# Performance work log

Hardware: AMD Instinct MI355X
Metric: run time of the kernel (lower is better)

The kernel has to match this reference:

```python
import jax, jax.numpy as jnp
import numpy as np

D_MODEL = 1024
EXPAND = 2
INNER = D_MODEL * EXPAND  # 2048
D_STATE = 64
K = 3
BSZ = 2
SEQ = 4096


def setup_inputs() -> dict:
    key = jax.random.key(0)
    ks = jax.random.split(key, 12)
    s = 0.02

    def w(k, shape):
        return jax.random.normal(k, shape, jnp.float32) * s

    return {
        "x": jax.random.normal(ks[0], (BSZ, SEQ, D_MODEL), jnp.float32),
        "W_in": w(ks[1], (D_MODEL, 2 * INNER)),
        "b_in": jnp.zeros((2 * INNER,), jnp.float32),
        "conv_w": w(ks[2], (INNER, K)),            # depthwise kernel per channel
        "conv_b": jnp.zeros((INNER,), jnp.float32),
        "W_dt": w(ks[3], (INNER, D_STATE)),
        "b_dt": jnp.zeros((D_STATE,), jnp.float32),
        "W_B": w(ks[4], (INNER, D_STATE)),
        "b_B": jnp.zeros((D_STATE,), jnp.float32),
        "W_C": w(ks[5], (INNER, D_STATE)),
        "b_C": jnp.zeros((D_STATE,), jnp.float32),
        "W_si": w(ks[6], (D_STATE, INNER)),
        "b_si": jnp.zeros((INNER,), jnp.float32),
        "D": jnp.ones((INNER,), jnp.float32),
        "W_out": w(ks[7], (INNER, D_MODEL)),
        "b_out": jnp.zeros((D_MODEL,), jnp.float32),
    }


def reference(x, W_in, b_in, conv_w, conv_b, W_dt, b_dt, W_B, b_B, W_C, b_C,
              W_si, b_si, D, W_out, b_out):
    bsz, seq_len, _ = x.shape
    inner = W_in.shape[1] // 2
    k = conv_w.shape[1]

    xz = x @ W_in + b_in                      # [B, L, 2*inner]
    x_main, gate = xz[..., :inner], xz[..., inner:]

    # Causal depthwise conv: torch pads k-1 both sides then slices [:L],
    # equivalent to left-pad (k-1), right-pad 0.
    lhs = jnp.transpose(x_main, (0, 2, 1))    # [B, C, L]
    rhs = conv_w[:, None, :]                  # [C, 1, K]
    conv = jax.lax.conv_general_dilated(
        lhs, rhs, window_strides=(1,), padding=[(k - 1, 0)],
        dimension_numbers=("NCH", "OIH", "NCH"), feature_group_count=inner)
    x_main = jnp.transpose(conv, (0, 2, 1)) + conv_b  # [B, L, inner]
    x_main = jax.nn.silu(x_main)

    dt = jax.nn.sigmoid(x_main @ W_dt + b_dt)  # [B, L, d_state]
    Bm = x_main @ W_B + b_B
    Cm = x_main @ W_C + b_C

    # Selective state recurrence: state_t = (1-dt_t)*state_{t-1} + dt_t*B_t
    def step(state, inp):
        dt_t, B_t, C_t = inp                  # each [B, d_state]
        state = (1.0 - dt_t) * state + dt_t * B_t
        return state, C_t * state

    xs = (jnp.moveaxis(dt, 1, 0), jnp.moveaxis(Bm, 1, 0), jnp.moveaxis(Cm, 1, 0))
    state0 = jnp.zeros((bsz, dt.shape[-1]), x.dtype)
    _, y = jax.lax.scan(step, state0, xs)     # [L, B, d_state]
    y = jnp.moveaxis(y, 0, 1)                 # [B, L, d_state]

    # LayerNorm over last dim, no affine, eps=1e-5 (torch F.layer_norm default)
    mu = jnp.mean(y, axis=-1, keepdims=True)
    var = jnp.var(y, axis=-1, keepdims=True)
    y = (y - mu) * jax.lax.rsqrt(var + 1e-5)

    y = y @ W_si + b_si                       # [B, L, inner]
    y = y + D * x_main
    y = y * jax.nn.sigmoid(gate)
    return y @ W_out + b_out                  # [B, L, d_model]
```

## Files before the change

### kernel.cpp

```cpp
#include <hip/hip_runtime.h>
#include <hip/hip_bf16.h>
#include <math.h>


namespace {

typedef __bf16 bf16x8 __attribute__((ext_vector_type(8)));
typedef float  f32x4  __attribute__((ext_vector_type(4)));
typedef unsigned short u16;

constexpr int kSeq = 4096;

__device__ __forceinline__ float sigmoid_f(float x) { return 1.0f / (1.0f + expf(-x)); }
__device__ __forceinline__ u16   f2bf(float f) { __bf16 h = (__bf16)f; return __builtin_bit_cast(u16, h); }
__device__ __forceinline__ float bf2f(u16 u)   { return (float)__builtin_bit_cast(__bf16, u); }

__device__ __forceinline__ void gll16(const u16* g, u16* l) {
    __builtin_amdgcn_global_load_lds(
        (const __attribute__((address_space(1))) unsigned int*)g,
        (__attribute__((address_space(3))) unsigned int*)l,
        16, 0, 0);
}

__device__ __forceinline__ int xcd_swizzle(int lin, int nwg) {
    const int q = nwg >> 3, r = nwg & 7;
    const int xcd = lin & 7, idx = lin >> 3;
    return (xcd < r ? xcd * (q + 1) : r * (q + 1) + (xcd - r) * q) + idx;
}

__global__ __launch_bounds__(256)
void convert_bf16(const float* __restrict__ in, u16* __restrict__ out, long n4)
{
    long i = (long)blockIdx.x * 256 + threadIdx.x;
    if (i >= n4) return;
    float4 v = reinterpret_cast<const float4*>(in)[i];
    ushort4 o = make_ushort4(f2bf(v.x), f2bf(v.y), f2bf(v.z), f2bf(v.w));
    reinterpret_cast<ushort4*>(out)[i] = o;
}

__device__ __forceinline__ void tr_body(float (*tile)[33],
                                        const float* __restrict__ in, u16* __restrict__ out,
                                        int R, int C, int r0, int c0, int t)
{
    const int lr = t >> 3, lc = (t & 7) * 4;
    float4 v = *reinterpret_cast<const float4*>(in + (size_t)(r0 + lr) * C + c0 + lc);
    tile[lr][lc + 0] = v.x; tile[lr][lc + 1] = v.y;
    tile[lr][lc + 2] = v.z; tile[lr][lc + 3] = v.w;
    __syncthreads();
    const int oc = t >> 3, orr = (t & 7) * 4;
    ushort4 o = make_ushort4(f2bf(tile[orr + 0][oc]), f2bf(tile[orr + 1][oc]),
                             f2bf(tile[orr + 2][oc]), f2bf(tile[orr + 3][oc]));
    *reinterpret_cast<ushort4*>(out + (size_t)(c0 + oc) * R + r0 + orr) = o;
}

__global__ __launch_bounds__(256)
void transpose_big(const float* __restrict__ Win, u16* __restrict__ WinT,
                   const float* __restrict__ Wout, u16* __restrict__ WoutT)
{
    __shared__ float tile[32][33];
    const int t = threadIdx.x;
    if (blockIdx.z == 0) {
        tr_body(tile, Win, WinT, 1024, 4096, blockIdx.y * 32, blockIdx.x * 32, t);
    } else {
        if (blockIdx.x >= 64) return;
        tr_body(tile, Wout, WoutT, 2048, 1024, blockIdx.x * 32, blockIdx.y * 32, t);
    }
}

__global__ __launch_bounds__(256)
void transpose_small(const float* __restrict__ Wdt, const float* __restrict__ WB,
                     const float* __restrict__ WC,  const float* __restrict__ Wsi,
                     u16* __restrict__ WdtbcT, u16* __restrict__ WsiT)
{
    __shared__ float tile[32][33];
    const int t = threadIdx.x;
    const int z = blockIdx.z;
    if (z < 3) {
        const float* in = (z == 0) ? Wdt : (z == 1) ? WB : WC;
        u16* out = WdtbcT + (size_t)z * 64 * 2048;
        tr_body(tile, in, out, 2048, 64, blockIdx.y * 32, blockIdx.x * 32, t);
    } else {
        tr_body(tile, Wsi, WsiT, 64, 2048, blockIdx.x * 32, blockIdx.y * 32, t);
    }
}

template <int BM, int BN, int EPI>
__global__ __launch_bounds__(256)
void gemm_mfma(const u16* __restrict__ A, const u16* __restrict__ Bt,
               const float* __restrict__ b0, const float* __restrict__ b1,
               const float* __restrict__ b2,
               const u16* __restrict__ aux0, const u16* __restrict__ aux1,
               void* __restrict__ o0, int N, int K, int nbx)
{
    constexpr int FM = BM / 32, FN = BN / 32;
    constexpr int CA = BM / 32, CB = BN / 32;
    __shared__ __align__(16) u16 As[BM][64];
    __shared__ __align__(16) u16 Bs[BN][64];

    const int tid  = threadIdx.x;
    const int lane = tid & 63;
    const int wid  = tid >> 6;
    const int wr   = (wid >> 1) * (BM / 2);
    const int wc   = (wid & 1)  * (BN / 2);
    const int swz  = xcd_swizzle(blockIdx.x, gridDim.x);
    const int row0 = (swz / nbx) * BM;
    const int col0 = (swz % nbx) * BN;

    const int srow = lane >> 3;
    const int scol = ((lane & 7) ^ srow) * 8;
    const int fr   = lane & 15;
    const int fq   = lane >> 4;

    f32x4 acc[FM][FN];
#pragma unroll
    for (int m = 0; m < FM; ++m)
#pragma unroll
        for (int n = 0; n < FN; ++n) acc[m][n] = (f32x4){0.f, 0.f, 0.f, 0.f};

    for (int k0 = 0; k0 < K; k0 += 64) {
#pragma unroll
        for (int i = 0; i < CA; ++i) {
            const int c = wid * CA + i;
            gll16(A + (size_t)(row0 + c * 8 + srow) * K + k0 + scol,
                  &As[0][0] + c * 512 + lane * 8);
        }
#pragma unroll
        for (int i = 0; i < CB; ++i) {
            const int c = wid * CB + i;
            gll16(Bt + (size_t)(col0 + c * 8 + srow) * K + k0 + scol,
                  &Bs[0][0] + c * 512 + lane * 8);
        }
        __syncthreads();
#pragma unroll
        for (int kk = 0; kk < 2; ++kk) {
            bf16x8 af[FM], bg[FN];
#pragma unroll
            for (int m = 0; m < FM; ++m) {
                const int rr = wr + m * 16 + fr;
                af[m] = *reinterpret_cast<const bf16x8*>(
                    &As[rr][(kk * 32 + fq * 8) ^ ((rr & 7) * 8)]);
            }
#pragma unroll
            for (int n = 0; n < FN; ++n) {
                const int rr = wc + n * 16 + fr;
                bg[n] = *reinterpret_cast<const bf16x8*>(
                    &Bs[rr][(kk * 32 + fq * 8) ^ ((rr & 7) * 8)]);
            }
#pragma unroll
            for (int m = 0; m < FM; ++m)
#pragma unroll
                for (int n = 0; n < FN; ++n)
                    acc[m][n] = __builtin_amdgcn_mfma_f32_16x16x32_bf16(af[m], bg[n], acc[m][n], 0, 0, 0);
        }
        __syncthreads();
    }

#pragma unroll
    for (int m = 0; m < FM; ++m) {
#pragma unroll
        for (int n = 0; n < FN; ++n) {
            const int gc  = col0 + wc + n * 16 + fr;
            const int gr0 = row0 + wr + m * 16 + fq * 4;
            if constexpr (EPI == 2) {
                float4 vv;
                float* vp = (float*)&vv;
#pragma unroll
                for (int j = 0; j < 4; ++j) {
                    float bb = (gc < 64) ? b0[gc] : (gc < 128) ? b1[gc - 64] : b2[gc - 128];
                    float v = acc[m][n][j] + bb;
                    if (gc < 64) v = sigmoid_f(v);
                    vp[j] = v;
                }
                *reinterpret_cast<float4*>(&((float*)o0)[(size_t)gc * 8192 + gr0]) = vv;
            } else {
#pragma unroll
                for (int j = 0; j < 4; ++j) {
                    const int gr = gr0 + j;
                    float v = acc[m][n][j];
                    if constexpr (EPI == 0) {
                        ((float*)o0)[(size_t)gr * N + gc] = v + b0[gc];
                    } else if constexpr (EPI == 1) {
                        ((u16*)o0)[(size_t)gr * N + gc] = f2bf(v + b0[gc]);
                    } else {
                        const size_t p = (size_t)gr * 2048 + gc;
                        float g  = bf2f(aux0[(size_t)gr * 4096 + gc]);
                        float xa = bf2f(aux1[p]);
                        v = v + b0[gc] + b1[gc] * xa;
                        ((u16*)o0)[p] = f2bf(v * sigmoid_f(g));
                    }
                }
            }
        }
    }
    (void)b1; (void)b2; (void)aux0; (void)aux1;
}

__global__ __launch_bounds__(256)
void conv_silu(const u16* __restrict__ xz, const float* __restrict__ cw,
               const float* __restrict__ cb, u16* __restrict__ xact)
{
    const size_t g  = ((size_t)blockIdx.x * 256 + threadIdx.x) * 8;
    const int    c0 = (int)(g & 2047);
    const size_t r  = g >> 11;
    const int    s  = (int)(r & (kSeq - 1));
    const u16* p = xz + r * 4096 + c0;
    u16 X0[8], X1[8] = {}, X2[8] = {};
    *reinterpret_cast<uint4*>(X0) = *reinterpret_cast<const uint4*>(p);
    if (s >= 1) *reinterpret_cast<uint4*>(X1) = *reinterpret_cast<const uint4*>(p - 4096);
    if (s >= 2) *reinterpret_cast<uint4*>(X2) = *reinterpret_cast<const uint4*>(p - 8192);
    u16 O[8];
#pragma unroll
    for (int j = 0; j < 8; ++j) {
        const int c = c0 + j;
        float v = bf2f(X2[j]) * cw[c * 3 + 0] + bf2f(X1[j]) * cw[c * 3 + 1]
                + bf2f(X0[j]) * cw[c * 3 + 2] + cb[c];
        O[j] = f2bf(v * sigmoid_f(v));
    }
    *reinterpret_cast<uint4*>(xact + r * 2048 + c0) = *reinterpret_cast<uint4*>(O);
}

__global__ __launch_bounds__(256)
void scan_kernel(const float* __restrict__ dtbcT, float* __restrict__ y)
{
    const int b = blockIdx.x >> 6;
    const int d = blockIdx.x & 63;
    const int t = threadIdx.x;
    const size_t col = (size_t)b * kSeq + t * 16;
    const float* dtp = dtbcT + (size_t)d         * 8192 + col;
    const float* Bp  = dtbcT + (size_t)(64 + d)  * 8192 + col;
    const float* Cp  = dtbcT + (size_t)(128 + d) * 8192 + col;

    float av[16], bv[16];
    float Acc = 1.f, Bcc = 0.f;
#pragma unroll
    for (int q = 0; q < 4; ++q) {
        float4 dv = *reinterpret_cast<const float4*>(dtp + q * 4);
        float4 Bv = *reinterpret_cast<const float4*>(Bp + q * 4);
        const float* dvp = (const float*)&dv;
        const float* bvp = (const float*)&Bv;
#pragma unroll
        for (int j = 0; j < 4; ++j) {
            const int i = q * 4 + j;
            float a  = 1.f - dvp[j];
            float bb = dvp[j] * bvp[j];
            av[i] = a; bv[i] = bb;
            Acc = a * Acc;
            Bcc = a * Bcc + bb;
        }
    }

    __shared__ float sA[256], sB[256];
    sA[t] = Acc; sB[t] = Bcc;
    __syncthreads();
    for (int off = 1; off < 256; off <<= 1) {
        float cA = sA[t], cB = sB[t];
        float pA = 1.f, pB = 0.f;
        if (t >= off) { pA = sA[t - off]; pB = sB[t - off]; }
        __syncthreads();
        if (t >= off) { sA[t] = cA * pA; sB[t] = cA * pB + cB; }
        __syncthreads();
    }

    float s = (t == 0) ? 0.f : sB[t - 1];
#pragma unroll
    for (int q = 0; q < 4; ++q) {
        float4 Cv = *reinterpret_cast<const float4*>(Cp + q * 4);
        const float* cvp = (const float*)&Cv;
#pragma unroll
        for (int j = 0; j < 4; ++j) {
            const int i = q * 4 + j;
            s = av[i] * s + bv[i];
            y[(col + i) * 64 + d] = cvp[j] * s;
        }
    }
}

__global__ __launch_bounds__(256)
void ln_kernel(const float* __restrict__ y, u16* __restrict__ ynb)
{
    const int w = threadIdx.x >> 6;
    const int l = threadIdx.x & 63;
    const size_t r = (size_t)blockIdx.x * 4 + w;
    float v  = y[r * 64 + l];
    float s  = v, s2 = v * v;
#pragma unroll
    for (int m = 1; m < 64; m <<= 1) {
        s  += __shfl_xor(s, m, 64);
        s2 += __shfl_xor(s2, m, 64);
    }
    float mu  = s * (1.f / 64.f);
    float var = s2 * (1.f / 64.f) - mu * mu;
    ynb[r * 64 + l] = f2bf((v - mu) * rsqrtf(var + 1e-5f));
}

}

extern "C" void kernel_launch(void* const* d_in, const int* in_sizes, int n_in,
                              void* d_out, int out_size, void* d_ws, size_t ws_size,
                              hipStream_t stream)
{
    (void)in_sizes; (void)n_in; (void)out_size; (void)ws_size;
    const float* x     = (const float*)d_in[0];
    const float* W_in  = (const float*)d_in[1];
    const float* b_in  = (const float*)d_in[2];
    const float* cw    = (const float*)d_in[3];
    const float* cb    = (const float*)d_in[4];
    const float* W_dt  = (const float*)d_in[5];
    const float* b_dt  = (const float*)d_in[6];
    const float* W_B   = (const float*)d_in[7];
    const float* b_B   = (const float*)d_in[8];
    const float* W_C   = (const float*)d_in[9];
    const float* b_C   = (const float*)d_in[10];
    const float* W_si  = (const float*)d_in[11];
    const float* b_si  = (const float*)d_in[12];
    const float* Dv    = (const float*)d_in[13];
    const float* W_out = (const float*)d_in[14];
    const float* b_out = (const float*)d_in[15];
    float* out = (float*)d_out;

    char* ws = (char*)d_ws;
    u16*   xzb    = (u16*)  (ws);
    u16*   xb     = (u16*)  (ws + 67108864);
    u16*   xact   = (u16*)  (ws + 83886080);
    u16*   hb     = (u16*)  (ws + 117440512);
    float* dtbcT  = (float*)(ws + 150994944);
    float* ybuf   = (float*)(ws + 157286400);
    u16*   ynb    = (u16*)  (ws + 159383552);
    u16*   WinT   = (u16*)  (ws + 160432128);
    u16*   WoutT  = (u16*)  (ws + 168820736);
    u16*   WdtbcT = (u16*)  (ws + 173015040);
    u16*   WsiT   = (u16*)  (ws + 173801472);

    dim3 blk(256);

    convert_bf16<<<dim3((8192L * 1024 / 4 + 255) / 256), blk, 0, stream>>>(x, xb, 8192L * 1024 / 4);
    transpose_big<<<dim3(128, 32, 2), blk, 0, stream>>>(W_in, WinT, W_out, WoutT);
    transpose_small<<<dim3(2, 64, 4), blk, 0, stream>>>(W_dt, W_B, W_C, W_si, WdtbcT, WsiT);

    gemm_mfma<128, 128, 1><<<dim3(32 * 64), blk, 0, stream>>>(
        xb, WinT, b_in, nullptr, nullptr, nullptr, nullptr, xzb, 4096, 1024, 32);
    conv_silu<<<dim3(8192L * 2048 / (8 * 256)), blk, 0, stream>>>(xzb, cw, cb, xact);
    gemm_mfma<64, 64, 2><<<dim3(3 * 128), blk, 0, stream>>>(
        xact, WdtbcT, b_dt, b_B, b_C, nullptr, nullptr, dtbcT, 192, 2048, 3);
    scan_kernel<<<dim3(128), blk, 0, stream>>>(dtbcT, ybuf);
    ln_kernel<<<dim3(8192 / 4), blk, 0, stream>>>(ybuf, ynb);
    gemm_mfma<128, 128, 3><<<dim3(16 * 64), blk, 0, stream>>>(
        ynb, WsiT, b_si, Dv, nullptr, xzb + 2048, xact, hb, 2048, 64, 16);
    gemm_mfma<128, 128, 0><<<dim3(8 * 64), blk, 0, stream>>>(
        hb, WoutT, b_out, nullptr, nullptr, nullptr, nullptr, out, 1024, 2048, 8);
}
```

Measured before the change: 237.8 us.

## Add double-buffered 256-tile GEMM, widen dt/B/C tile, warp-shuffle scan

Adds a 512-thread GEMM kernel with 256-wide tiles, double-buffered LDS filled by global_load_lds, and four interleaved phases of loads and MFMAs separated by barriers and priority hints. The input and output projections now use it. The dt/B/C projection uses one 64x192 tile per row block instead of three 64x64 tiles. The scan's block-level prefix now uses wavefront shuffles plus a small cross-wave combine instead of a barrier-heavy LDS loop. The aim is better MFMA utilisation and latency hiding in the large GEMMs and fewer synchronisations in the scan. The cost is more LDS and register pressure and lower occupancy. gemm_mfma's epilogue is reduced to the EPI 3 path, so the EPI 2 instance and code paths are what remain in that template.

```diff
diff --git a/kernel.cpp b/kernel.cpp
--- a/kernel.cpp
+++ b/kernel.cpp
@@ -84,6 +84,148 @@
     }
 }
 
+#define PHASE(PH, MH, NH, RDA, RDB)                                           \
+  {                                                                           \
+    if (t + 1 < nt) {                                                         \
+      _Pragma("unroll")                                                       \
+      for (int i = 0; i < NCA + NCB; ++i) {                                   \
+        if ((i * 4) / (NCA + NCB) == (PH)) {                                  \
+          if (i < NCA) {                                                      \
+            const int ca = wid * NCA + i;                                     \
+            gll16(A + (size_t)(row0 + ca * 8 + srow) * K + knext + scol,      \
+                  abase_n + ca * 512 + lane * 8);                             \
+          } else {                                                            \
+            const int cb = wid * NCB + (i - NCA);                             \
+            gll16(Bt + (size_t)(col0 + cb * 8 + srow) * K + knext + scol,     \
+                  bbase_n + cb * 512 + lane * 8);                             \
+          }                                                                   \
+        }                                                                     \
+      }                                                                       \
+    }                                                                         \
+    if (RDA) {                                                                \
+      _Pragma("unroll")                                                       \
+      for (int m = 0; m < FMH; ++m) {                                         \
+        const int rr = wr + ((MH) * FMH + m) * 16 + fr;                       \
+        _Pragma("unroll")                                                     \
+        for (int kk = 0; kk < 2; ++kk)                                        \
+          af[m][kk] = *reinterpret_cast<const bf16x8*>(                       \
+              abase_c + rr * 64 + (((kk * 4 + fq) ^ (rr & 7)) * 8));          \
+      }                                                                       \
+    }                                                                         \
+    if (RDB) {                                                                \
+      _Pragma("unroll")                                                       \
+      for (int n = 0; n < FNH; ++n) {                                         \
+        const int rr = wc + ((NH) * FNH + n) * 16 + fr;                       \
+        _Pragma("unroll")                                                     \
+        for (int kk = 0; kk < 2; ++kk)                                        \
+          bg[n][kk] = *reinterpret_cast<const bf16x8*>(                       \
+              bbase_c + rr * 64 + (((kk * 4 + fq) ^ (rr & 7)) * 8));          \
+      }                                                                       \
+    }                                                                         \
+    __builtin_amdgcn_s_barrier();                                             \
+    __builtin_amdgcn_s_setprio(1);                                            \
+    _Pragma("unroll")                                                         \
+    for (int m = 0; m < FMH; ++m)                                             \
+      _Pragma("unroll")                                                       \
+      for (int n = 0; n < FNH; ++n)                                           \
+        _Pragma("unroll")                                                     \
+        for (int kk = 0; kk < 2; ++kk)                                        \
+          acc[(MH) * FMH + m][(NH) * FNH + n] =                               \
+              __builtin_amdgcn_mfma_f32_16x16x32_bf16(                        \
+                  af[m][kk], bg[n][kk], acc[(MH) * FMH + m][(NH) * FNH + n],  \
+                  0, 0, 0);                                                   \
+    __builtin_amdgcn_s_setprio(0);                                            \
+    __builtin_amdgcn_s_barrier();                                             \
+  }
+
+template <int BM, int BN, int WM, int WN, int EPI>
+__global__ __launch_bounds__(512, 2)
+void gemm256(const u16* __restrict__ A, const u16* __restrict__ Bt,
+             const float* __restrict__ b0, void* __restrict__ o0,
+             int N, int K, int nbx)
+{
+    constexpr int WTM = BM / WM, WTN = BN / WN;
+    constexpr int FM  = WTM / 16, FN = WTN / 16;
+    constexpr int FMH = FM / 2,  FNH = FN / 2;
+    constexpr int NCA = BM / 64, NCB = BN / 64;
+
+    __shared__ __align__(16) u16 As[2][BM * 64];
+    __shared__ __align__(16) u16 Bs[2][BN * 64];
+
+    const int tid  = threadIdx.x;
+    const int lane = tid & 63;
+    const int wid  = tid >> 6;
+    const int wr   = (wid / WN) * WTM;
+    const int wc   = (wid % WN) * WTN;
+    const int swz  = xcd_swizzle(blockIdx.x, gridDim.x);
+    const int row0 = (swz / nbx) * BM;
+    const int col0 = (swz % nbx) * BN;
+
+    const int srow = lane >> 3;
+    const int scol = ((lane & 7) ^ srow) * 8;
+    const int fr   = lane & 15;
+    const int fq   = lane >> 4;
+
+    const int nt = K / 64;
+
+    f32x4 acc[FM][FN];
+#pragma unroll
+    for (int m = 0; m < FM; ++m)
+#pragma unroll
+        for (int n = 0; n < FN; ++n) acc[m][n] = (f32x4){0.f, 0.f, 0.f, 0.f};
+
+#pragma unroll
+    for (int i = 0; i < NCA + NCB; ++i) {
+        if (i < NCA) {
+            const int ca = wid * NCA + i;
+            gll16(A + (size_t)(row0 + ca * 8 + srow) * K + scol,
+                  &As[0][0] + ca * 512 + lane * 8);
+        } else {
+            const int cb = wid * NCB + (i - NCA);
+            gll16(Bt + (size_t)(col0 + cb * 8 + srow) * K + scol,
+                  &Bs[0][0] + cb * 512 + lane * 8);
+        }
+    }
+    __syncthreads();
+
+    bf16x8 af[FMH][2], bg[FNH][2];
+
+    for (int t = 0; t < nt; ++t) {
+        const int cur = t & 1;
+        u16* abase_c = &As[cur][0];
+        u16* bbase_c = &Bs[cur][0];
+        u16* abase_n = &As[cur ^ 1][0];
+        u16* bbase_n = &Bs[cur ^ 1][0];
+        const int knext = (t + 1) * 64;
+
+        PHASE(0, 0, 0, true,  true)
+        PHASE(1, 0, 1, false, true)
+        PHASE(2, 1, 1, true,  false)
+        PHASE(3, 1, 0, false, true)
+
+        __syncthreads();
+    }
+
+#pragma unroll
+    for (int m = 0; m < FM; ++m) {
+#pragma unroll
+        for (int n = 0; n < FN; ++n) {
+            const int gc  = col0 + wc + n * 16 + fr;
+            const int gr0 = row0 + wr + m * 16 + fq * 4;
+#pragma unroll
+            for (int j = 0; j < 4; ++j) {
+                const float v = acc[m][n][j] + b0[gc];
+                if constexpr (EPI == 0) {
+                    ((float*)o0)[(size_t)(gr0 + j) * N + gc] = v;
+                } else {
+                    ((u16*)o0)[(size_t)(gr0 + j) * N + gc] = f2bf(v);
+                }
+            }
+        }
+    }
+}
+#undef PHASE
+
 template <int BM, int BN, int EPI>
 __global__ __launch_bounds__(256)
 void gemm_mfma(const u16* __restrict__ A, const u16* __restrict__ Bt,
@@ -176,18 +318,11 @@
 #pragma unroll
                 for (int j = 0; j < 4; ++j) {
                     const int gr = gr0 + j;
-                    float v = acc[m][n][j];
-                    if constexpr (EPI == 0) {
-                        ((float*)o0)[(size_t)gr * N + gc] = v + b0[gc];
-                    } else if constexpr (EPI == 1) {
-                        ((u16*)o0)[(size_t)gr * N + gc] = f2bf(v + b0[gc]);
-                    } else {
-                        const size_t p = (size_t)gr * 2048 + gc;
-                        float g  = bf2f(aux0[(size_t)gr * 4096 + gc]);
-                        float xa = bf2f(aux1[p]);
-                        v = v + b0[gc] + b1[gc] * xa;
-                        ((u16*)o0)[p] = f2bf(v * sigmoid_f(g));
-                    }
+                    const size_t p = (size_t)gr * 2048 + gc;
+                    float g  = bf2f(aux0[(size_t)gr * 4096 + gc]);
+                    float xa = bf2f(aux1[p]);
+                    float v = acc[m][n][j] + b0[gc] + b1[gc] * xa;
+                    ((u16*)o0)[p] = f2bf(v * sigmoid_f(g));
                 }
             }
         }
@@ -225,6 +360,8 @@
     const int b = blockIdx.x >> 6;
     const int d = blockIdx.x & 63;
     const int t = threadIdx.x;
+    const int lane = t & 63;
+    const int w = t >> 6;
     const size_t col = (size_t)b * kSeq + t * 16;
     const float* dtp = dtbcT + (size_t)d         * 8192 + col;
     const float* Bp  = dtbcT + (size_t)(64 + d)  * 8192 + col;
@@ -249,19 +386,22 @@
         }
     }
 
-    __shared__ float sA[256], sB[256];
-    sA[t] = Acc; sB[t] = Bcc;
+#pragma unroll
+    for (int off = 1; off < 64; off <<= 1) {
+        float pA = __shfl_up(Acc, off, 64);
+        float pB = __shfl_up(Bcc, off, 64);
+        if (lane >= off) { Bcc = Acc * pB + Bcc; Acc = Acc * pA; }
+    }
+    __shared__ float wA[4], wB[4];
+    if (lane == 63) { wA[w] = Acc; wB[w] = Bcc; }
+    float eA = __shfl_up(Acc, 1, 64);
+    float eB = __shfl_up(Bcc, 1, 64);
+    if (lane == 0) { eA = 1.f; eB = 0.f; }
     __syncthreads();
-    for (int off = 1; off < 256; off <<= 1) {
-        float cA = sA[t], cB = sB[t];
-        float pA = 1.f, pB = 0.f;
-        if (t >= off) { pA = sA[t - off]; pB = sB[t - off]; }
-        __syncthreads();
-        if (t >= off) { sA[t] = cA * pA; sB[t] = cA * pB + cB; }
-        __syncthreads();
-    }
-
-    float s = (t == 0) ? 0.f : sB[t - 1];
+    float sW = 0.f;
+    for (int i = 0; i < w; ++i) sW = wA[i] * sW + wB[i];
+    float s = eA * sW + eB;
+
 #pragma unroll
     for (int q = 0; q < 4; ++q) {
         float4 Cv = *reinterpret_cast<const float4*>(Cp + q * 4);
@@ -332,20 +472,21 @@
     u16*   WsiT   = (u16*)  (ws + 173801472);
 
     dim3 blk(256);
+    dim3 blk512(512);
 
     convert_bf16<<<dim3((8192L * 1024 / 4 + 255) / 256), blk, 0, stream>>>(x, xb, 8192L * 1024 / 4);
     transpose_big<<<dim3(128, 32, 2), blk, 0, stream>>>(W_in, WinT, W_out, WoutT);
     transpose_small<<<dim3(2, 64, 4), blk, 0, stream>>>(W_dt, W_B, W_C, W_si, WdtbcT, WsiT);
 
-    gemm_mfma<128, 128, 1><<<dim3(32 * 64), blk, 0, stream>>>(
-        xb, WinT, b_in, nullptr, nullptr, nullptr, nullptr, xzb, 4096, 1024, 32);
+    gemm256<256, 256, 2, 4, 1><<<dim3(32 * 16), blk512, 0, stream>>>(
+        xb, WinT, b_in, xzb, 4096, 1024, 16);
     conv_silu<<<dim3(8192L * 2048 / (8 * 256)), blk, 0, stream>>>(xzb, cw, cb, xact);
-    gemm_mfma<64, 64, 2><<<dim3(3 * 128), blk, 0, stream>>>(
-        xact, WdtbcT, b_dt, b_B, b_C, nullptr, nullptr, dtbcT, 192, 2048, 3);
+    gemm_mfma<64, 192, 2><<<dim3(128), blk, 0, stream>>>(
+        xact, WdtbcT, b_dt, b_B, b_C, nullptr, nullptr, dtbcT, 192, 2048, 1);
     scan_kernel<<<dim3(128), blk, 0, stream>>>(dtbcT, ybuf);
     ln_kernel<<<dim3(8192 / 4), blk, 0, stream>>>(ybuf, ynb);
     gemm_mfma<128, 128, 3><<<dim3(16 * 64), blk, 0, stream>>>(
         ynb, WsiT, b_si, Dv, nullptr, xzb + 2048, xact, hb, 2048, 64, 16);
-    gemm_mfma<128, 128, 0><<<dim3(8 * 64), blk, 0, stream>>>(
-        hb, WoutT, b_out, nullptr, nullptr, nullptr, nullptr, out, 1024, 2048, 8);
-}
+    gemm256<256, 128, 4, 2, 0><<<dim3(32 * 8), blk512, 0, stream>>>(
+        hb, WoutT, b_out, out, 1024, 2048, 8);
+}
```

Measured after the change: 310.3 us. 1.3x slower.

## Merge preprocessing kernels and use 8-wave GEMM blocks for large projections

Applied to the files above, without the earlier changes.

Folds the input bf16 conversion and all weight transposes into a single prep kernel, cutting two kernel launches. Generalises the MFMA GEMM template over the wave grid, and launches the in-projection and out-projection GEMMs with 512-thread blocks (2x4 waves) plus a min-waves launch bound. Each wave then holds fewer accumulator fragments, which is meant to raise occupancy and latency hiding. The trade-off is more waves sharing each loaded tile and possible register caps under the new launch bounds.

```diff
diff --git a/kernel.cpp b/kernel.cpp
--- a/kernel.cpp
+++ b/kernel.cpp
@@ -26,16 +26,6 @@
     const int q = nwg >> 3, r = nwg & 7;
     const int xcd = lin & 7, idx = lin >> 3;
     return (xcd < r ? xcd * (q + 1) : r * (q + 1) + (xcd - r) * q) + idx;
-}
-
-__global__ __launch_bounds__(256)
-void convert_bf16(const float* __restrict__ in, u16* __restrict__ out, long n4)
-{
-    long i = (long)blockIdx.x * 256 + threadIdx.x;
-    if (i >= n4) return;
-    float4 v = reinterpret_cast<const float4*>(in)[i];
-    ushort4 o = make_ushort4(f2bf(v.x), f2bf(v.y), f2bf(v.z), f2bf(v.w));
-    reinterpret_cast<ushort4*>(out)[i] = o;
 }
 
 __device__ __forceinline__ void tr_body(float (*tile)[33],
@@ -54,54 +44,64 @@
 }
 
 __global__ __launch_bounds__(256)
-void transpose_big(const float* __restrict__ Win, u16* __restrict__ WinT,
-                   const float* __restrict__ Wout, u16* __restrict__ WoutT)
-{
+void prep_all(const float* __restrict__ x,    u16* __restrict__ xb,
+              const float* __restrict__ Win,  u16* __restrict__ WinT,
+              const float* __restrict__ Wout, u16* __restrict__ WoutT,
+              const float* __restrict__ Wdt,  const float* __restrict__ WB,
+              const float* __restrict__ WC,   u16* __restrict__ WdtbcT,
+              const float* __restrict__ Wsi,  u16* __restrict__ WsiT)
+{
+    const int t = threadIdx.x;
+    int b = blockIdx.x;
+    if (b < 8192) {
+        long i = (long)b * 256 + t;
+        float4 v = reinterpret_cast<const float4*>(x)[i];
+        ushort4 o = make_ushort4(f2bf(v.x), f2bf(v.y), f2bf(v.z), f2bf(v.w));
+        reinterpret_cast<ushort4*>(xb)[i] = o;
+        return;
+    }
     __shared__ float tile[32][33];
-    const int t = threadIdx.x;
-    if (blockIdx.z == 0) {
-        tr_body(tile, Win, WinT, 1024, 4096, blockIdx.y * 32, blockIdx.x * 32, t);
-    } else {
-        if (blockIdx.x >= 64) return;
-        tr_body(tile, Wout, WoutT, 2048, 1024, blockIdx.x * 32, blockIdx.y * 32, t);
-    }
-}
-
-__global__ __launch_bounds__(256)
-void transpose_small(const float* __restrict__ Wdt, const float* __restrict__ WB,
-                     const float* __restrict__ WC,  const float* __restrict__ Wsi,
-                     u16* __restrict__ WdtbcT, u16* __restrict__ WsiT)
-{
-    __shared__ float tile[32][33];
-    const int t = threadIdx.x;
-    const int z = blockIdx.z;
-    if (z < 3) {
+    b -= 8192;
+    if (b < 4096) {
+        tr_body(tile, Win, WinT, 1024, 4096, (b / 128) * 32, (b % 128) * 32, t);
+        return;
+    }
+    b -= 4096;
+    if (b < 2048) {
+        tr_body(tile, Wout, WoutT, 2048, 1024, (b % 64) * 32, (b / 64) * 32, t);
+        return;
+    }
+    b -= 2048;
+    if (b < 384) {
+        const int z = b / 128, rem = b % 128;
         const float* in = (z == 0) ? Wdt : (z == 1) ? WB : WC;
-        u16* out = WdtbcT + (size_t)z * 64 * 2048;
-        tr_body(tile, in, out, 2048, 64, blockIdx.y * 32, blockIdx.x * 32, t);
-    } else {
-        tr_body(tile, Wsi, WsiT, 64, 2048, blockIdx.x * 32, blockIdx.y * 32, t);
-    }
-}
-
-template <int BM, int BN, int EPI>
-__global__ __launch_bounds__(256)
+        u16* outp = WdtbcT + (size_t)z * 64 * 2048;
+        tr_body(tile, in, outp, 2048, 64, (rem / 2) * 32, (rem % 2) * 32, t);
+        return;
+    }
+    b -= 384;
+    tr_body(tile, Wsi, WsiT, 64, 2048, (b % 2) * 32, (b / 2) * 32, t);
+}
+
+template <int BM, int BN, int WM, int WN, int MINW, int EPI>
+__global__ __launch_bounds__(WM * WN * 64, MINW)
 void gemm_mfma(const u16* __restrict__ A, const u16* __restrict__ Bt,
                const float* __restrict__ b0, const float* __restrict__ b1,
                const float* __restrict__ b2,
                const u16* __restrict__ aux0, const u16* __restrict__ aux1,
                void* __restrict__ o0, int N, int K, int nbx)
 {
-    constexpr int FM = BM / 32, FN = BN / 32;
-    constexpr int CA = BM / 32, CB = BN / 32;
+    constexpr int WAVES = WM * WN;
+    constexpr int FM = BM / WM / 16, FN = BN / WN / 16;
+    constexpr int CA = BM / (8 * WAVES), CB = BN / (8 * WAVES);
     __shared__ __align__(16) u16 As[BM][64];
     __shared__ __align__(16) u16 Bs[BN][64];
 
     const int tid  = threadIdx.x;
     const int lane = tid & 63;
     const int wid  = tid >> 6;
-    const int wr   = (wid >> 1) * (BM / 2);
-    const int wc   = (wid & 1)  * (BN / 2);
+    const int wr   = (wid / WN) * (BM / WM);
+    const int wc   = (wid % WN) * (BN / WN);
     const int swz  = xcd_swizzle(blockIdx.x, gridDim.x);
     const int row0 = (swz / nbx) * BM;
     const int col0 = (swz % nbx) * BN;
@@ -332,20 +332,20 @@
     u16*   WsiT   = (u16*)  (ws + 173801472);
 
     dim3 blk(256);
-
-    convert_bf16<<<dim3((8192L * 1024 / 4 + 255) / 256), blk, 0, stream>>>(x, xb, 8192L * 1024 / 4);
-    transpose_big<<<dim3(128, 32, 2), blk, 0, stream>>>(W_in, WinT, W_out, WoutT);
-    transpose_small<<<dim3(2, 64, 4), blk, 0, stream>>>(W_dt, W_B, W_C, W_si, WdtbcT, WsiT);
-
-    gemm_mfma<128, 128, 1><<<dim3(32 * 64), blk, 0, stream>>>(
+    dim3 blk512(512);
+
+    prep_all<<<dim3(8192 + 4096 + 2048 + 384 + 128), blk, 0, stream>>>(
+        x, xb, W_in, WinT, W_out, WoutT, W_dt, W_B, W_C, WdtbcT, W_si, WsiT);
+
+    gemm_mfma<128, 128, 2, 4, 4, 1><<<dim3(32 * 64), blk512, 0, stream>>>(
         xb, WinT, b_in, nullptr, nullptr, nullptr, nullptr, xzb, 4096, 1024, 32);
     conv_silu<<<dim3(8192L * 2048 / (8 * 256)), blk, 0, stream>>>(xzb, cw, cb, xact);
-    gemm_mfma<64, 64, 2><<<dim3(3 * 128), blk, 0, stream>>>(
+    gemm_mfma<64, 64, 2, 2, 1, 2><<<dim3(3 * 128), blk, 0, stream>>>(
         xact, WdtbcT, b_dt, b_B, b_C, nullptr, nullptr, dtbcT, 192, 2048, 3);
     scan_kernel<<<dim3(128), blk, 0, stream>>>(dtbcT, ybuf);
     ln_kernel<<<dim3(8192 / 4), blk, 0, stream>>>(ybuf, ynb);
-    gemm_mfma<128, 128, 3><<<dim3(16 * 64), blk, 0, stream>>>(
+    gemm_mfma<128, 128, 2, 2, 1, 3><<<dim3(16 * 64), blk, 0, stream>>>(
         ynb, WsiT, b_si, Dv, nullptr, xzb + 2048, xact, hb, 2048, 64, 16);
-    gemm_mfma<128, 128, 0><<<dim3(8 * 64), blk, 0, stream>>>(
+    gemm_mfma<128, 128, 2, 4, 4, 0><<<dim3(8 * 64), blk512, 0, stream>>>(
         hb, WoutT, b_out, nullptr, nullptr, nullptr, nullptr, out, 1024, 2048, 8);
 }
```

Result: faster. 232.2 us (-2.4%).
